# Kernel optimization log

Hardware: AMD Instinct MI355X
Metric: run time of the kernel (lower is better)

Reference implementation:

```python
import jax, jax.numpy as jnp
import numpy as np

N, E, G = 100000, 300000, 4096
ND, ED, H, ZI, ZS, NE, L = 64, 16, 256, 128, 128, 8, 3
LAMBDA_GRL = 1.0


def setup_inputs() -> dict:
    key = jax.random.key(0)
    ks = iter(jax.random.split(key, 64))
    def nrm(shape, scale=0.05):
        return jax.random.normal(next(ks), shape, jnp.float32) * scale
    inp = {
        'x': jax.random.normal(next(ks), (N, ND), jnp.float32),
        'edge_index': jax.random.randint(next(ks), (2, E), 0, N),
        'edge_attr': jax.random.normal(next(ks), (E, ED), jnp.float32),
        'batch': jnp.sort(jax.random.randint(next(ks), (N,), 0, G)),
        'node_W': nrm((ND, H)), 'node_b': nrm((H,)),
        'conv_eps': jnp.zeros((L,), jnp.float32),
        'edge_W': nrm((L, ED, H)), 'edge_b': nrm((L, H)),
        'mlp_W1': nrm((L, H, H)), 'mlp_b1': nrm((L, H)),
        'mlp_W2': nrm((L, H, H)), 'mlp_b2': nrm((L, H)),
        'gn_w': jnp.ones((L, H), jnp.float32), 'gn_b': jnp.zeros((L, H), jnp.float32),
        'gn_ms': jnp.ones((L, H), jnp.float32),
        'finv_W1': nrm((H, ZI)), 'finv_b1': nrm((ZI,)),
        'finv_W2': nrm((ZI, ZI)), 'finv_b2': nrm((ZI,)),
        'fspu_W1': nrm((H, ZS)), 'fspu_b1': nrm((ZS,)),
        'fspu_W2': nrm((ZS, ZS)), 'fspu_b2': nrm((ZS,)),
        'pred_W1': nrm((ZI, ZI)), 'pred_b1': nrm((ZI,)),
        'pred_W2': nrm((ZI, 1)), 'pred_b2': nrm((1,)),
        'adv_W1': nrm((ZI, ZI)), 'adv_b1': nrm((ZI,)),
        'adv_W2': nrm((ZI, NE)), 'adv_b2': nrm((NE,)),
    }
    return inp


def _mlp2(h, W1, b1, W2, b2):
    return jax.nn.relu(h @ W1 + b1) @ W2 + b2


def reference(x, edge_index, edge_attr, batch, node_W, node_b, conv_eps,
              edge_W, edge_b, mlp_W1, mlp_b1, mlp_W2, mlp_b2,
              gn_w, gn_b, gn_ms,
              finv_W1, finv_b1, finv_W2, finv_b2,
              fspu_W1, fspu_b1, fspu_W2, fspu_b2,
              pred_W1, pred_b1, pred_W2, pred_b2,
              adv_W1, adv_b1, adv_W2, adv_b2):
    src, dst = edge_index[0], edge_index[1]
    cnt = jax.ops.segment_sum(jnp.ones((N, 1), jnp.float32), batch, num_segments=G)
    cnt = jnp.maximum(cnt, 1.0)
    h = x @ node_W + node_b  # [N,H]
    for l in range(L):
        # GINEConv: sum_j relu(x_j + lin(e_ij))
        e = edge_attr @ edge_W[l] + edge_b[l]            # [E,H]
        m = jax.nn.relu(h[src] + e)                      # [E,H]
        agg = jax.ops.segment_sum(m, dst, num_segments=N)
        h = _mlp2((1.0 + conv_eps[l]) * h + agg, mlp_W1[l], mlp_b1[l], mlp_W2[l], mlp_b2[l])
        # GraphNorm
        mean = jax.ops.segment_sum(h, batch, num_segments=G) / cnt  # [G,H]
        out = h - gn_ms[l] * mean[batch]
        var = jax.ops.segment_sum(out * out, batch, num_segments=G) / cnt
        h = out * jax.lax.rsqrt(var[batch] + 1e-5) * gn_w[l] + gn_b[l]
        h = jax.nn.relu(h)  # dropout is identity at eval
    hg = jax.ops.segment_sum(h, batch, num_segments=G) / cnt  # global_mean_pool [G,H]
    z_inv = _mlp2(hg, finv_W1, finv_b1, finv_W2, finv_b2)
    z_spu = _mlp2(hg, fspu_W1, fspu_b1, fspu_W2, fspu_b2)
    yhat = _mlp2(z_inv, pred_W1, pred_b1, pred_W2, pred_b2)[:, 0]
    # gradient reversal: identity fwd, -lambda on bwd
    grl = jax.lax.stop_gradient(z_inv) * (1.0 + LAMBDA_GRL) - LAMBDA_GRL * z_inv
    envhat = _mlp2(grl, adv_W1, adv_b1, adv_W2, adv_b2)
    return (hg, z_inv, z_spu, yhat, envhat)
```

## Files before the change

kernel.cpp:

```cpp
#include <hip/hip_runtime.h>
#include <hip/hip_bf16.h>

typedef __bf16 bf16_t;
typedef __bf16 bf16x8 __attribute__((ext_vector_type(8)));
typedef __bf16 bf16x4 __attribute__((ext_vector_type(4)));
typedef float  f32x4  __attribute__((ext_vector_type(4)));

static constexpr int N_NODES = 100000;
static constexpr int N_EDGES = 300000;
static constexpr int N_GRAPH = 4096;
static constexpr int H  = 256;
static constexpr int ND = 64;
static constexpr int ZIC = 128;
static constexpr int NE = 8;
static constexpr int SCAN_B = 1024;

__device__ __forceinline__ int clampi(int v, int lo, int hi) {
  return v < lo ? lo : (v > hi ? hi : v);
}

__device__ __forceinline__ void dma16(const bf16_t* g, bf16_t* lds_base) {
  __builtin_amdgcn_global_load_lds(
      (const __attribute__((address_space(1))) void*)g,
      (__attribute__((address_space(3))) void*)lds_base, 16, 0, 0);
}

__global__ void compute_starts_kernel(const int* __restrict__ batch,
                                      int* __restrict__ starts,
                                      int* __restrict__ counts,
                                      int* __restrict__ cursor, int N, int G) {
  int i = blockIdx.x * blockDim.x + threadIdx.x;
  if (i >= N) return;
  counts[i] = 0;
  cursor[i] = 0;
  int b = clampi(batch[i], 0, G - 1);
  if (i == 0) {
    for (int g = 0; g <= b; ++g) starts[g] = 0;
  } else {
    int p = clampi(batch[i - 1], 0, G - 1);
    for (int g = p + 1; g <= b; ++g) starts[g] = i;
  }
  if (i == N - 1) {
    for (int g = b + 1; g <= G; ++g) starts[g] = N;
  }
}

__global__ void count_deg_kernel(const int* __restrict__ dst, int* __restrict__ counts, int E, int N) {
  int e = blockIdx.x * blockDim.x + threadIdx.x;
  if (e < E) atomicAdd(&counts[clampi(dst[e], 0, N - 1)], 1);
}

__global__ __launch_bounds__(SCAN_B) void scan1_kernel(const int* __restrict__ counts,
                                                       int* __restrict__ offs,
                                                       int* __restrict__ bsum, int N) {
  __shared__ int tmp[SCAN_B];
  int i = blockIdx.x * SCAN_B + threadIdx.x;
  int v = (i < N) ? counts[i] : 0;
  tmp[threadIdx.x] = v;
  __syncthreads();
  for (int d = 1; d < SCAN_B; d <<= 1) {
    int t = (threadIdx.x >= d) ? tmp[threadIdx.x - d] : 0;
    __syncthreads();
    tmp[threadIdx.x] += t;
    __syncthreads();
  }
  if (i < N) offs[i + 1] = tmp[threadIdx.x];
  if (threadIdx.x == SCAN_B - 1) bsum[blockIdx.x] = tmp[SCAN_B - 1];
  if (i == 0) offs[0] = 0;
}

__global__ void scan2_kernel(int* __restrict__ bsum, int nblk) {
  if (blockIdx.x == 0 && threadIdx.x == 0) {
    int run = 0;
    for (int b = 0; b < nblk; ++b) { int v = bsum[b]; bsum[b] = run; run += v; }
  }
}

__global__ __launch_bounds__(SCAN_B) void scan3_kernel(int* __restrict__ offs,
                                                       const int* __restrict__ bsum, int N) {
  int i = blockIdx.x * SCAN_B + threadIdx.x;
  if (i < N) offs[i + 1] += bsum[blockIdx.x];
}

__global__ void fill_scatter_kernel(const int* __restrict__ src, const int* __restrict__ dst,
                                    const float* __restrict__ eattr,
                                    const int* __restrict__ offs, int* __restrict__ cursor,
                                    int* __restrict__ src_srt, bf16_t* __restrict__ eat16,
                                    int E, int N) {
  int e = blockIdx.x * blockDim.x + threadIdx.x;
  if (e >= E) return;
  int d = clampi(dst[e], 0, N - 1);
  int pos = offs[d] + atomicAdd(&cursor[d], 1);
  if ((unsigned)pos >= (unsigned)E) return;
  int s = src[e];
  src_srt[pos] = ((unsigned)s < (unsigned)N_NODES) ? s : 0;
  const float* ea = eattr + (size_t)e * 16;
  union { bf16_t b[16]; uint4 u[2]; } pk;
#pragma unroll
  for (int k = 0; k < 16; ++k) pk.b[k] = (bf16_t)ea[k];
  uint4* dst16 = (uint4*)(eat16 + ((size_t)pos << 4));
  dst16[0] = pk.u[0];
  dst16[1] = pk.u[1];
}

__global__ void build_ewt16_kernel(const float* __restrict__ edge_W,
                                   bf16_t* __restrict__ ewt) {
  int idx = blockIdx.x * blockDim.x + threadIdx.x;
  if (idx >= 3 * 256 * 16) return;
  int l = idx / (256 * 16);
  int rem = idx - l * 256 * 16;
  int n = rem >> 4, k = rem & 15;
  ewt[idx] = (bf16_t)edge_W[(size_t)l * 16 * 256 + k * 256 + n];
}

__global__ void transpose_kernel(const float* __restrict__ W,
                                 bf16_t* __restrict__ Wt, int K, int Nc,
                                 size_t srcStride, size_t dstStride) {
  __shared__ float tile[32][33];
  const float* Wz = W + (size_t)blockIdx.z * srcStride;
  bf16_t* Wtz = Wt + (size_t)blockIdx.z * dstStride;
  int n0 = blockIdx.x * 32, k0 = blockIdx.y * 32;
  int tx = threadIdx.x, ty = threadIdx.y;
  for (int i = ty; i < 32; i += 8)
    tile[i][tx] = Wz[(size_t)(k0 + i) * Nc + n0 + tx];
  __syncthreads();
  for (int i = ty; i < 32; i += 8)
    Wtz[(size_t)(n0 + i) * K + k0 + tx] = (bf16_t)tile[tx][i];
}

__device__ __forceinline__ void load8_to_lds(const bf16_t* p, bool valid, uint4* dst) {
  uint4 v = make_uint4(0u, 0u, 0u, 0u);
  if (valid) v = *(const uint4*)p;
  *dst = v;
}
__device__ __forceinline__ void load8_to_lds(const float* p, bool valid, uint4* dst) {
  float4 f0 = make_float4(0.f, 0.f, 0.f, 0.f), f1 = f0;
  if (valid) { f0 = *(const float4*)p; f1 = *(const float4*)(p + 4); }
  union { bf16_t b[8]; uint4 u; } pk;
  pk.b[0] = (bf16_t)f0.x; pk.b[1] = (bf16_t)f0.y;
  pk.b[2] = (bf16_t)f0.z; pk.b[3] = (bf16_t)f0.w;
  pk.b[4] = (bf16_t)f1.x; pk.b[5] = (bf16_t)f1.y;
  pk.b[6] = (bf16_t)f1.z; pk.b[7] = (bf16_t)f1.w;
  *dst = pk.u;
}

template<int K, bool RELU, bool OUTF32, typename TIN>
__global__ __launch_bounds__(256) void gemm128_kernel(
    const TIN* __restrict__ U, const bf16_t* __restrict__ Wt,
    const float* __restrict__ bias, void* __restrict__ Out, int M, int Nc) {
  constexpr int LDT = 72;
  __shared__ bf16_t Ut[128 * LDT];
  __shared__ bf16_t Wl[128 * LDT];
  const int m0 = blockIdx.x * 128;
  const int n0 = blockIdx.y * 128;
  const int t = threadIdx.x;
  const int lane = t & 63;
  const int wave = t >> 6;
  const int wm = (wave >> 1) * 64;
  const int wn = (wave & 1) * 64;
  const int srow = t >> 1;
  const int sk = (t & 1) * 32;
  const int lr = lane & 15;
  const int lq = lane >> 4;
  const bool aok = (m0 + srow) < M;
  f32x4 acc[4][4] = {};

  for (int k0 = 0; k0 < K; k0 += 64) {
    const TIN* up = U + (size_t)(m0 + srow) * K + k0 + sk;
    const bf16_t* wp = Wt + (size_t)(n0 + srow) * K + k0 + sk;
#pragma unroll
    for (int q = 0; q < 4; ++q) {
      load8_to_lds(up + q * 8, aok, (uint4*)&Ut[srow * LDT + sk + q * 8]);
      load8_to_lds(wp + q * 8, true, (uint4*)&Wl[srow * LDT + sk + q * 8]);
    }
    __syncthreads();
#pragma unroll
    for (int s = 0; s < 2; ++s) {
      bf16x8 a[4], b[4];
#pragma unroll
      for (int mt = 0; mt < 4; ++mt)
        a[mt] = *(const bf16x8*)(&Ut[(wm + mt * 16 + lr) * LDT + s * 32 + lq * 8]);
#pragma unroll
      for (int nt = 0; nt < 4; ++nt)
        b[nt] = *(const bf16x8*)(&Wl[(wn + nt * 16 + lr) * LDT + s * 32 + lq * 8]);
#pragma unroll
      for (int mt = 0; mt < 4; ++mt)
#pragma unroll
        for (int nt = 0; nt < 4; ++nt)
          acc[mt][nt] = __builtin_amdgcn_mfma_f32_16x16x32_bf16(
              a[mt], b[nt], acc[mt][nt], 0, 0, 0);
    }
    __syncthreads();
  }

#pragma unroll
  for (int mt = 0; mt < 4; ++mt)
#pragma unroll
    for (int nt = 0; nt < 4; ++nt) {
      int col = n0 + wn + nt * 16 + lr;
      float bcol = bias[col];
#pragma unroll
      for (int r = 0; r < 4; ++r) {
        int row = m0 + wm + mt * 16 + lq * 4 + r;
        if (row < M) {
          float vv = acc[mt][nt][r] + bcol;
          if (RELU) vv = vv > 0.f ? vv : 0.f;
          if (OUTF32) ((float*)Out)[(size_t)row * Nc + col] = vv;
          else        ((bf16_t*)Out)[(size_t)row * Nc + col] = (bf16_t)vv;
        }
      }
    }
}

template<int K, bool RELU, bool OUTF32, typename TIN>
__global__ __launch_bounds__(256) void gemm64x2_kernel(
    const TIN* __restrict__ U0, const bf16_t* __restrict__ Wt0,
    const float* __restrict__ b0, void* __restrict__ O0,
    const TIN* __restrict__ U1, const bf16_t* __restrict__ Wt1,
    const float* __restrict__ b1, void* __restrict__ O1, int M, int Nc) {
  constexpr int LDT = 72;
  __shared__ bf16_t Ut[64 * LDT];
  __shared__ bf16_t Wl[64 * LDT];
  const TIN*    U    = blockIdx.z ? U1 : U0;
  const bf16_t* Wt   = blockIdx.z ? Wt1 : Wt0;
  const float*  bias = blockIdx.z ? b1 : b0;
  void*         Out  = blockIdx.z ? O1 : O0;
  const int m0 = blockIdx.x * 64;
  const int n0 = blockIdx.y * 64;
  const int t = threadIdx.x;
  const int lane = t & 63;
  const int wave = t >> 6;
  const int wm = (wave >> 1) * 32;
  const int wn = (wave & 1) * 32;
  const int srow = t >> 2;
  const int sk = (t & 3) * 8;
  const int lr = lane & 15;
  const int lq = lane >> 4;
  const bool aok = (m0 + srow) < M;
  f32x4 acc[2][2] = {};

  for (int k0 = 0; k0 < K; k0 += 64) {
    const TIN* up = U + (size_t)(m0 + srow) * K + k0 + sk;
    const bf16_t* wp = Wt + (size_t)(n0 + srow) * K + k0 + sk;
    load8_to_lds(up,      aok, (uint4*)&Ut[srow * LDT + sk]);
    load8_to_lds(up + 32, aok, (uint4*)&Ut[srow * LDT + sk + 32]);
    load8_to_lds(wp,      true, (uint4*)&Wl[srow * LDT + sk]);
    load8_to_lds(wp + 32, true, (uint4*)&Wl[srow * LDT + sk + 32]);
    __syncthreads();
#pragma unroll
    for (int s = 0; s < 2; ++s) {
      bf16x8 a[2], b[2];
#pragma unroll
      for (int mt = 0; mt < 2; ++mt)
        a[mt] = *(const bf16x8*)(&Ut[(wm + mt * 16 + lr) * LDT + s * 32 + lq * 8]);
#pragma unroll
      for (int nt = 0; nt < 2; ++nt)
        b[nt] = *(const bf16x8*)(&Wl[(wn + nt * 16 + lr) * LDT + s * 32 + lq * 8]);
#pragma unroll
      for (int mt = 0; mt < 2; ++mt)
#pragma unroll
        for (int nt = 0; nt < 2; ++nt)
          acc[mt][nt] = __builtin_amdgcn_mfma_f32_16x16x32_bf16(
              a[mt], b[nt], acc[mt][nt], 0, 0, 0);
    }
    __syncthreads();
  }

#pragma unroll
  for (int mt = 0; mt < 2; ++mt)
#pragma unroll
    for (int nt = 0; nt < 2; ++nt) {
      int col = n0 + wn + nt * 16 + lr;
      float bcol = bias[col];
#pragma unroll
      for (int r = 0; r < 4; ++r) {
        int row = m0 + wm + mt * 16 + lq * 4 + r;
        if (row < M) {
          float vv = acc[mt][nt][r] + bcol;
          if (RELU) vv = vv > 0.f ? vv : 0.f;
          if (OUTF32) ((float*)Out)[(size_t)row * Nc + col] = vv;
          else        ((bf16_t*)Out)[(size_t)row * Nc + col] = (bf16_t)vv;
        }
      }
    }
}

template<int K, bool RELU, bool OUTF32>
__global__ __launch_bounds__(256) void gemm128_dma_kernel(
    const bf16_t* __restrict__ U, const bf16_t* __restrict__ Wt,
    const float* __restrict__ bias, void* __restrict__ Out, int M, int Nc) {
  __shared__ bf16_t Ut[128 * 64];
  __shared__ bf16_t Wl[128 * 64];
  const int t = threadIdx.x;
  const int lane = t & 63;
  const int wave = t >> 6;
  const int m0 = blockIdx.x * 128;
  const int n0 = blockIdx.y * 128;
  const int wm = (wave >> 1) * 64;
  const int wn = (wave & 1) * 64;
  const int lr = lane & 15;
  const int lq = lane >> 4;
  const int subrow = wave * 8 + (lane >> 3);
  const int lchunk = (lane & 7) ^ (lane >> 3);
  f32x4 acc[4][4] = {};

  for (int k0 = 0; k0 < K; k0 += 64) {
#pragma unroll
    for (int q = 0; q < 4; ++q) {
      const int row = q * 32 + subrow;
      int urow = m0 + row; if (urow >= M) urow = M - 1;
      dma16(U + (size_t)urow * K + k0 + lchunk * 8, &Ut[(q * 32 + wave * 8) * 64]);
      dma16(Wt + (size_t)(n0 + row) * K + k0 + lchunk * 8, &Wl[(q * 32 + wave * 8) * 64]);
    }
    __syncthreads();
#pragma unroll
    for (int s = 0; s < 2; ++s) {
      bf16x8 a[4], b[4];
#pragma unroll
      for (int mt = 0; mt < 4; ++mt)
        a[mt] = *(const bf16x8*)(&Ut[(wm + mt * 16 + lr) * 64 + (((s * 4 + lq) ^ (lr & 7)) << 3)]);
#pragma unroll
      for (int nt = 0; nt < 4; ++nt)
        b[nt] = *(const bf16x8*)(&Wl[(wn + nt * 16 + lr) * 64 + (((s * 4 + lq) ^ (lr & 7)) << 3)]);
#pragma unroll
      for (int mt = 0; mt < 4; ++mt)
#pragma unroll
        for (int nt = 0; nt < 4; ++nt)
          acc[mt][nt] = __builtin_amdgcn_mfma_f32_16x16x32_bf16(
              a[mt], b[nt], acc[mt][nt], 0, 0, 0);
    }
    __syncthreads();
  }

#pragma unroll
  for (int mt = 0; mt < 4; ++mt)
#pragma unroll
    for (int nt = 0; nt < 4; ++nt) {
      int col = n0 + wn + nt * 16 + lr;
      float bcol = bias[col];
#pragma unroll
      for (int r = 0; r < 4; ++r) {
        int row = m0 + wm + mt * 16 + lq * 4 + r;
        if (row < M) {
          float vv = acc[mt][nt][r] + bcol;
          if (RELU) vv = vv > 0.f ? vv : 0.f;
          if (OUTF32) ((float*)Out)[(size_t)row * Nc + col] = vv;
          else        ((bf16_t*)Out)[(size_t)row * Nc + col] = (bf16_t)vv;
        }
      }
    }
}

__global__ __launch_bounds__(256) void gine_gather_mfma_kernel(
    const bf16_t* __restrict__ h, const bf16_t* __restrict__ eat16,
    const int* __restrict__ src_sorted, const int* __restrict__ offs,
    const bf16_t* __restrict__ ewt, const float* __restrict__ eb,
    const float* __restrict__ eps_p, bf16_t* __restrict__ u) {
  constexpr int HP = H + 8;
  __shared__ bf16_t slin[2][16 * HP];
  const int t = threadIdx.x;
  const int wave = t >> 6;
  const int lane = t & 63;
  const int lr = lane & 15;
  const int lq = lane >> 4;
  const int lane4 = lane * 4;
  const int n0 = blockIdx.x * 16;
  const int nodeB = n0 + wave * 4;

  bf16x4 hs[4];
#pragma unroll
  for (int k = 0; k < 4; ++k)
    hs[k] = *(const bf16x4*)(h + (size_t)(nodeB + k) * H + lane4);

  bf16x8 bfrag[4];
#pragma unroll
  for (int nt = 0; nt < 4; ++nt) {
    bf16x8 bv = {};
    if (lq < 2)
      bv = *(const bf16x8*)(ewt + ((wave * 64 + nt * 16 + lr) << 4) + (lq << 3));
    bfrag[nt] = bv;
  }
  float ebv[4];
#pragma unroll
  for (int i = 0; i < 4; ++i) ebv[i] = eb[lane4 + i];

  int bs = offs[n0], be = offs[n0 + 16];
  bs = clampi(bs, 0, N_EDGES);
  be = clampi(be, bs, N_EDGES);
  int nb[5];
#pragma unroll
  for (int q = 0; q < 5; ++q) nb[q] = offs[nodeB + q];
  nb[0] = clampi(nb[0], bs, be);
#pragma unroll
  for (int q = 1; q < 5; ++q) nb[q] = clampi(nb[q], nb[q - 1], be);

  f32x4 accv[4] = {};
  int parity = 0;

  for (int cb = bs; cb < be; cb += 16, parity ^= 1) {
    int arow = cb + lr;
    if (arow >= N_EDGES) arow = N_EDGES - 1;
    bf16x8 afrag = {};
    if (lq < 2)
      afrag = *(const bf16x8*)(eat16 + ((size_t)arow << 4) + (lq << 3));

    int j0p = nb[0] > cb ? nb[0] : cb;
    int j1p = nb[1] < cb + 16 ? nb[1] : cb + 16;
    int sidx[4];
    bf16x4 hv[4];
    if (j0p < j1p) {
#pragma unroll
      for (int q = 0; q < 4; ++q) {
        int jj = j0p + q; if (jj > j1p - 1) jj = j1p - 1;
        sidx[q] = src_sorted[jj];
      }
    }

    f32x4 c[4];
#pragma unroll
    for (int nt = 0; nt < 4; ++nt) {
      f32x4 z = {};
      c[nt] = __builtin_amdgcn_mfma_f32_16x16x32_bf16(afrag, bfrag[nt], z, 0, 0, 0);
    }
#pragma unroll
    for (int nt = 0; nt < 4; ++nt)
#pragma unroll
      for (int r = 0; r < 4; ++r)
        slin[parity][(lq * 4 + r) * HP + wave * 64 + nt * 16 + lr] = (bf16_t)c[nt][r];

    if (j0p < j1p) {
#pragma unroll
      for (int q = 0; q < 4; ++q)
        hv[q] = *(const bf16x4*)(h + (size_t)sidx[q] * H + lane4);
    }

    __syncthreads();

#pragma unroll
    for (int k = 0; k < 4; ++k) {
      int j0 = nb[k] > cb ? nb[k] : cb;
      int j1 = nb[k + 1] < cb + 16 ? nb[k + 1] : cb + 16;
      for (int jb = j0; jb < j1; jb += 4) {
        if (k != 0 || jb != j0p) {
#pragma unroll
          for (int q = 0; q < 4; ++q) {
            int jj = jb + q; if (jj > j1 - 1) jj = j1 - 1;
            sidx[q] = src_sorted[jj];
          }
#pragma unroll
          for (int q = 0; q < 4; ++q)
            hv[q] = *(const bf16x4*)(h + (size_t)sidx[q] * H + lane4);
        }
#pragma unroll
        for (int q = 0; q < 4; ++q) {
          if (jb + q < j1) {
            bf16x4 lv = *(const bf16x4*)(&slin[parity][(jb + q - cb) * HP + lane4]);
#pragma unroll
            for (int i = 0; i < 4; ++i)
              accv[k][i] += fmaxf((float)hv[q][i] + (float)lv[i] + ebv[i], 0.f);
          }
        }
      }
    }
  }

  const float sc = 1.0f + eps_p[0];
#pragma unroll
  for (int k = 0; k < 4; ++k) {
    union { bf16x4 v; uint2 b; } o;
#pragma unroll
    for (int i = 0; i < 4; ++i) o.v[i] = (bf16_t)(sc * (float)hs[k][i] + accv[k][i]);
    *(uint2*)(u + (size_t)(nodeB + k) * H + lane4) = o.b;
  }
}

__global__ __launch_bounds__(256) void graphnorm_kernel(
    const bf16_t* __restrict__ v, bf16_t* __restrict__ hout,
    const int* __restrict__ starts,
    const float* __restrict__ w, const float* __restrict__ b,
    const float* __restrict__ ms, float* __restrict__ hg) {
  constexpr int RS = 9;
  constexpr int PS = 13;
  __shared__ float red[4 * 64 * RS];
  __shared__ float prm[64 * PS];
  const int g = blockIdx.x;
  const int t = threadIdx.x;
  const int lane = t & 63;
  const int wave = t >> 6;
  const int c0 = lane * 4;
  int s = starts[g], e = starts[g + 1];
  s = clampi(s, 0, N_NODES);
  e = clampi(e, s, N_NODES);
  const float cnt = (float)((e - s) > 1 ? (e - s) : 1);

  float sx[4] = {0.f, 0.f, 0.f, 0.f}, sxx[4] = {0.f, 0.f, 0.f, 0.f};
  {
    int i = s + wave;
    for (; i + 4 < e; i += 8) {
      bf16x4 x0 = *(const bf16x4*)(v + (size_t)i * H + c0);
      bf16x4 x1 = *(const bf16x4*)(v + (size_t)(i + 4) * H + c0);
#pragma unroll
      for (int j = 0; j < 4; ++j) {
        float f0 = (float)x0[j], f1 = (float)x1[j];
        sx[j] += f0 + f1; sxx[j] += f0 * f0 + f1 * f1;
      }
    }
    if (i < e) {
      bf16x4 x0 = *(const bf16x4*)(v + (size_t)i * H + c0);
#pragma unroll
      for (int j = 0; j < 4; ++j) {
        float f0 = (float)x0[j];
        sx[j] += f0; sxx[j] += f0 * f0;
      }
    }
  }
  float* myred = &red[(wave * 64 + lane) * RS];
#pragma unroll
  for (int j = 0; j < 4; ++j) { myred[j] = sx[j]; myred[4 + j] = sxx[j]; }
  __syncthreads();

  if (wave == 0) {
#pragma unroll
    for (int j = 0; j < 4; ++j) {
      float fsx = red[lane * RS + j] + red[(64 + lane) * RS + j] +
                  red[(128 + lane) * RS + j] + red[(192 + lane) * RS + j];
      float fsxx = red[lane * RS + 4 + j] + red[(64 + lane) * RS + 4 + j] +
                   red[(128 + lane) * RS + 4 + j] + red[(192 + lane) * RS + 4 + j];
      float mean = fsx / cnt;
      float sub = ms[c0 + j] * mean;
      float var = fsxx / cnt - 2.f * sub * mean + sub * sub;
      var = fmaxf(var, 0.f);
      prm[lane * PS + j] = sub;
      prm[lane * PS + 4 + j] = rsqrtf(var + 1e-5f) * w[c0 + j];
      prm[lane * PS + 8 + j] = b[c0 + j];
    }
  }
  __syncthreads();
  float sub[4], inv[4], bb[4];
#pragma unroll
  for (int j = 0; j < 4; ++j) {
    sub[j] = prm[lane * PS + j];
    inv[j] = prm[lane * PS + 4 + j];
    bb[j] = prm[lane * PS + 8 + j];
  }

  float psum[4] = {0.f, 0.f, 0.f, 0.f};
  {
    int i = s + wave;
    for (; i + 4 < e; i += 8) {
      bf16x4 x0 = *(const bf16x4*)(v + (size_t)i * H + c0);
      bf16x4 x1 = *(const bf16x4*)(v + (size_t)(i + 4) * H + c0);
      union { bf16x4 o; uint2 u; } p0, p1;
#pragma unroll
      for (int j = 0; j < 4; ++j) {
        float o0 = ((float)x0[j] - sub[j]) * inv[j] + bb[j];
        float o1 = ((float)x1[j] - sub[j]) * inv[j] + bb[j];
        o0 = o0 > 0.f ? o0 : 0.f;
        o1 = o1 > 0.f ? o1 : 0.f;
        psum[j] += o0 + o1;
        p0.o[j] = (bf16_t)o0; p1.o[j] = (bf16_t)o1;
      }
      *(uint2*)(hout + (size_t)i * H + c0) = p0.u;
      *(uint2*)(hout + (size_t)(i + 4) * H + c0) = p1.u;
    }
    if (i < e) {
      bf16x4 x0 = *(const bf16x4*)(v + (size_t)i * H + c0);
      union { bf16x4 o; uint2 u; } p0;
#pragma unroll
      for (int j = 0; j < 4; ++j) {
        float o0 = ((float)x0[j] - sub[j]) * inv[j] + bb[j];
        o0 = o0 > 0.f ? o0 : 0.f;
        psum[j] += o0;
        p0.o[j] = (bf16_t)o0;
      }
      *(uint2*)(hout + (size_t)i * H + c0) = p0.u;
    }
  }

  if (hg) {
#pragma unroll
    for (int j = 0; j < 4; ++j) myred[j] = psum[j];
    __syncthreads();
    if (wave == 0) {
#pragma unroll
      for (int j = 0; j < 4; ++j) {
        float p = red[lane * RS + j] + red[(64 + lane) * RS + j] +
                  red[(128 + lane) * RS + j] + red[(192 + lane) * RS + j];
        hg[(size_t)g * H + c0 + j] = p / cnt;
      }
    }
  }
}

__global__ void head_out2_kernel(const bf16_t* __restrict__ In1, const float* __restrict__ W1,
                                 const float* __restrict__ b1, float* __restrict__ O1,
                                 const bf16_t* __restrict__ In2, const float* __restrict__ W2,
                                 const float* __restrict__ b2, float* __restrict__ O2,
                                 int M) {
  int idx = blockIdx.x * blockDim.x + threadIdx.x;
  if (idx < M) {
    float acc = b1[0];
    const bf16_t* in = In1 + (size_t)idx * ZIC;
    for (int k = 0; k < ZIC; ++k) acc += (float)in[k] * W1[k];
    O1[idx] = acc;
  } else {
    int j = idx - M;
    if (j >= M * NE) return;
    int r = j >> 3, n = j & 7;
    float acc = b2[n];
    const bf16_t* in = In2 + (size_t)r * ZIC;
    for (int k = 0; k < ZIC; ++k) acc += (float)in[k] * W2[(size_t)k * NE + n];
    O2[j] = acc;
  }
}

extern "C" void kernel_launch(void* const* d_in, const int* in_sizes, int n_in,
                              void* d_out, int out_size, void* d_ws, size_t ws_size,
                              hipStream_t stream) {
  (void)in_sizes; (void)n_in; (void)out_size; (void)ws_size;
  const float* x        = (const float*)d_in[0];
  const int*   eidx     = (const int*)d_in[1];
  const float* eattr    = (const float*)d_in[2];
  const int*   batch    = (const int*)d_in[3];
  const float* node_W   = (const float*)d_in[4];
  const float* node_b   = (const float*)d_in[5];
  const float* conv_eps = (const float*)d_in[6];
  const float* edge_W   = (const float*)d_in[7];
  const float* edge_b   = (const float*)d_in[8];
  const float* mlp_W1   = (const float*)d_in[9];
  const float* mlp_b1   = (const float*)d_in[10];
  const float* mlp_W2   = (const float*)d_in[11];
  const float* mlp_b2   = (const float*)d_in[12];
  const float* gn_w     = (const float*)d_in[13];
  const float* gn_b     = (const float*)d_in[14];
  const float* gn_ms    = (const float*)d_in[15];
  const float* finv_W1  = (const float*)d_in[16];
  const float* finv_b1  = (const float*)d_in[17];
  const float* finv_W2  = (const float*)d_in[18];
  const float* finv_b2  = (const float*)d_in[19];
  const float* fspu_W1  = (const float*)d_in[20];
  const float* fspu_b1  = (const float*)d_in[21];
  const float* fspu_W2  = (const float*)d_in[22];
  const float* fspu_b2  = (const float*)d_in[23];
  const float* pred_W1  = (const float*)d_in[24];
  const float* pred_b1  = (const float*)d_in[25];
  const float* pred_W2  = (const float*)d_in[26];
  const float* pred_b2  = (const float*)d_in[27];
  const float* adv_W1   = (const float*)d_in[28];
  const float* adv_b1   = (const float*)d_in[29];
  const float* adv_W2   = (const float*)d_in[30];
  const float* adv_b2   = (const float*)d_in[31];
  float* out = (float*)d_out;

  float* out_hg = out;
  float* out_zi = out + (size_t)N_GRAPH * H;
  float* out_zs = out_zi + (size_t)N_GRAPH * ZIC;
  float* out_yh = out_zs + (size_t)N_GRAPH * ZIC;
  float* out_ev = out_yh + N_GRAPH;

  char* wp = (char*)d_ws;
  auto alloc = [&](size_t bytes) { char* p = wp; wp += (bytes + 255) & ~(size_t)255; return p; };
  bf16_t* A        = (bf16_t*)alloc((size_t)N_NODES * H * 2);
  bf16_t* B        = (bf16_t*)alloc((size_t)N_NODES * H * 2);
  bf16_t* Wt       = (bf16_t*)alloc((size_t)(H * ND + 6 * H * H) * 2);
  bf16_t* WtH      = (bf16_t*)alloc((size_t)(2 * ZIC * H + 4 * ZIC * ZIC) * 2);
  bf16_t* ewt16    = (bf16_t*)alloc((size_t)3 * 256 * 16 * 2);
  bf16_t* eat16    = (bf16_t*)alloc((size_t)N_EDGES * 16 * 2);
  int*    starts   = (int*)alloc((size_t)(N_GRAPH + 1) * 4);
  int*    counts   = (int*)alloc((size_t)N_NODES * 4);
  int*    cursor   = (int*)alloc((size_t)N_NODES * 4);
  int*    offs     = (int*)alloc((size_t)(N_NODES + 1) * 4);
  int*    bsum     = (int*)alloc((size_t)SCAN_B * 4);
  int*    src_srt  = (int*)alloc((size_t)N_EDGES * 4);
  bf16_t* tmp1     = (bf16_t*)alloc((size_t)N_GRAPH * ZIC * 2);
  bf16_t* tmp2     = (bf16_t*)alloc((size_t)N_GRAPH * ZIC * 2);

  const int* srcp = eidx;
  const int* dstp = eidx + N_EDGES;
  const int nscan = (N_NODES + SCAN_B - 1) / SCAN_B;

  compute_starts_kernel<<<(N_NODES + 255) / 256, 256, 0, stream>>>(
      batch, starts, counts, cursor, N_NODES, N_GRAPH);
  count_deg_kernel<<<(N_EDGES + 255) / 256, 256, 0, stream>>>(dstp, counts, N_EDGES, N_NODES);
  scan1_kernel<<<nscan, SCAN_B, 0, stream>>>(counts, offs, bsum, N_NODES);
  scan2_kernel<<<1, 64, 0, stream>>>(bsum, nscan);
  scan3_kernel<<<nscan, SCAN_B, 0, stream>>>(offs, bsum, N_NODES);
  fill_scatter_kernel<<<(N_EDGES + 255) / 256, 256, 0, stream>>>(
      srcp, dstp, eattr, offs, cursor, src_srt, eat16, N_EDGES, N_NODES);
  build_ewt16_kernel<<<(3 * 256 * 16 + 255) / 256, 256, 0, stream>>>(edge_W, ewt16);

  bf16_t* WtN = Wt;
  bf16_t* Wt1base = Wt + H * ND;
  bf16_t* Wt2base = Wt + H * ND + (size_t)H * H;
  auto Wt1l = [&](int l) { return Wt1base + (size_t)(2 * l) * H * H; };
  auto Wt2l = [&](int l) { return Wt2base + (size_t)(2 * l) * H * H; };
  transpose_kernel<<<dim3(H / 32, ND / 32, 1), dim3(32, 8), 0, stream>>>(node_W, WtN, ND, H, 0, 0);
  transpose_kernel<<<dim3(H / 32, H / 32, 3), dim3(32, 8), 0, stream>>>(
      mlp_W1, Wt1base, H, H, (size_t)H * H, (size_t)2 * H * H);
  transpose_kernel<<<dim3(H / 32, H / 32, 3), dim3(32, 8), 0, stream>>>(
      mlp_W2, Wt2base, H, H, (size_t)H * H, (size_t)2 * H * H);

  bf16_t* fT1 = WtH;
  bf16_t* fT2 = fT1 + ZIC * H;
  bf16_t* sT1 = fT2 + ZIC * ZIC;
  bf16_t* sT2 = sT1 + ZIC * H;
  bf16_t* pT1 = sT2 + ZIC * ZIC;
  bf16_t* aT1 = pT1 + ZIC * ZIC;
  transpose_kernel<<<dim3(ZIC / 32, H / 32, 1), dim3(32, 8), 0, stream>>>(finv_W1, fT1, H, ZIC, 0, 0);
  transpose_kernel<<<dim3(ZIC / 32, ZIC / 32, 1), dim3(32, 8), 0, stream>>>(finv_W2, fT2, ZIC, ZIC, 0, 0);
  transpose_kernel<<<dim3(ZIC / 32, H / 32, 1), dim3(32, 8), 0, stream>>>(fspu_W1, sT1, H, ZIC, 0, 0);
  transpose_kernel<<<dim3(ZIC / 32, ZIC / 32, 1), dim3(32, 8), 0, stream>>>(fspu_W2, sT2, ZIC, ZIC, 0, 0);
  transpose_kernel<<<dim3(ZIC / 32, ZIC / 32, 1), dim3(32, 8), 0, stream>>>(pred_W1, pT1, ZIC, ZIC, 0, 0);
  transpose_kernel<<<dim3(ZIC / 32, ZIC / 32, 1), dim3(32, 8), 0, stream>>>(adv_W1, aT1, ZIC, ZIC, 0, 0);

  dim3 ggrid((N_NODES + 127) / 128, H / 128);
  gemm128_kernel<ND, false, false><<<ggrid, 256, 0, stream>>>(x, WtN, node_b, A, N_NODES, H);

  for (int l = 0; l < 3; ++l) {
    gine_gather_mfma_kernel<<<N_NODES / 16, 256, 0, stream>>>(
        A, eat16, src_srt, offs, ewt16 + (size_t)l * 256 * 16,
        edge_b + l * H, conv_eps + l, B);
    gemm128_dma_kernel<H, true,  false><<<ggrid, 256, 0, stream>>>(B, Wt1l(l), mlp_b1 + l * H, A, N_NODES, H);
    gemm128_dma_kernel<H, false, false><<<ggrid, 256, 0, stream>>>(A, Wt2l(l), mlp_b2 + l * H, B, N_NODES, H);
    graphnorm_kernel<<<N_GRAPH, 256, 0, stream>>>(B, A, starts, gn_w + l * H, gn_b + l * H,
                                                  gn_ms + l * H, (l == 2) ? out_hg : nullptr);
  }

  dim3 hgrid2(N_GRAPH / 64, ZIC / 64, 2);
  gemm64x2_kernel<H, true, false, float><<<hgrid2, 256, 0, stream>>>(
      out_hg, fT1, finv_b1, tmp1, out_hg, sT1, fspu_b1, tmp2, N_GRAPH, ZIC);
  gemm64x2_kernel<ZIC, false, true, bf16_t><<<hgrid2, 256, 0, stream>>>(
      tmp1, fT2, finv_b2, out_zi, tmp2, sT2, fspu_b2, out_zs, N_GRAPH, ZIC);
  gemm64x2_kernel<ZIC, true, false, float><<<hgrid2, 256, 0, stream>>>(
      out_zi, pT1, pred_b1, tmp1, out_zi, aT1, adv_b1, tmp2, N_GRAPH, ZIC);
  head_out2_kernel<<<(N_GRAPH * (1 + NE) + 255) / 256, 256, 0, stream>>>(
      tmp1, pred_W2, pred_b2, out_yh, tmp2, adv_W2, adv_b2, out_ev, N_GRAPH);
}
```

Measured before the change: 836.8 us.

## Make GINE gather per-wave independent, removing block-wide syncs via per-wave edge-linear LDS

Each wave now computes the full 256-wide edge linear projection for its own 4 nodes' edge range into a private LDS slice, so the block-wide __syncthreads per 16-edge chunk disappears and waves iterate only over their own edges. The edge weight table is permuted so each lane's MFMA output columns land contiguously and can be packed into 8-byte LDS stores. The cost is four times as many MFMAs per wave (the full H instead of a quarter), B fragments reloaded from global/L1 each chunk, and more LDS.

```diff
diff --git a/kernel.cpp b/kernel.cpp
--- a/kernel.cpp
+++ b/kernel.cpp
@@ -109,8 +109,9 @@
   if (idx >= 3 * 256 * 16) return;
   int l = idx / (256 * 16);
   int rem = idx - l * 256 * 16;
-  int n = rem >> 4, k = rem & 15;
-  ewt[idx] = (bf16_t)edge_W[(size_t)l * 16 * 256 + k * 256 + n];
+  int s = rem >> 4, k = rem & 15;
+  int ch = ((s & 15) << 4) | (s >> 4);
+  ewt[idx] = (bf16_t)edge_W[(size_t)l * 16 * 256 + k * 256 + ch];
 }
 
 __global__ void transpose_kernel(const float* __restrict__ W,
@@ -356,85 +357,76 @@
     const int* __restrict__ src_sorted, const int* __restrict__ offs,
     const bf16_t* __restrict__ ewt, const float* __restrict__ eb,
     const float* __restrict__ eps_p, bf16_t* __restrict__ u) {
-  constexpr int HP = H + 8;
-  __shared__ bf16_t slin[2][16 * HP];
+  constexpr int HPS = 264;
+  __shared__ bf16_t slin[4][16 * HPS];
   const int t = threadIdx.x;
   const int wave = t >> 6;
   const int lane = t & 63;
   const int lr = lane & 15;
   const int lq = lane >> 4;
   const int lane4 = lane * 4;
-  const int n0 = blockIdx.x * 16;
-  const int nodeB = n0 + wave * 4;
+  const int nodeB = blockIdx.x * 16 + wave * 4;
+  bf16_t* sl = &slin[wave][0];
 
   bf16x4 hs[4];
 #pragma unroll
   for (int k = 0; k < 4; ++k)
     hs[k] = *(const bf16x4*)(h + (size_t)(nodeB + k) * H + lane4);
 
-  bf16x8 bfrag[4];
-#pragma unroll
-  for (int nt = 0; nt < 4; ++nt) {
-    bf16x8 bv = {};
-    if (lq < 2)
-      bv = *(const bf16x8*)(ewt + ((wave * 64 + nt * 16 + lr) << 4) + (lq << 3));
-    bfrag[nt] = bv;
-  }
   float ebv[4];
 #pragma unroll
   for (int i = 0; i < 4; ++i) ebv[i] = eb[lane4 + i];
 
-  int bs = offs[n0], be = offs[n0 + 16];
-  bs = clampi(bs, 0, N_EDGES);
-  be = clampi(be, bs, N_EDGES);
   int nb[5];
 #pragma unroll
   for (int q = 0; q < 5; ++q) nb[q] = offs[nodeB + q];
-  nb[0] = clampi(nb[0], bs, be);
-#pragma unroll
-  for (int q = 1; q < 5; ++q) nb[q] = clampi(nb[q], nb[q - 1], be);
+  nb[0] = clampi(nb[0], 0, N_EDGES);
+#pragma unroll
+  for (int q = 1; q < 5; ++q) nb[q] = clampi(nb[q], nb[q - 1], N_EDGES);
 
   f32x4 accv[4] = {};
-  int parity = 0;
-
-  for (int cb = bs; cb < be; cb += 16, parity ^= 1) {
+
+  for (int cb = nb[0]; cb < nb[4]; cb += 16) {
+    int j0p = nb[0] > cb ? nb[0] : cb;
+    int j1p = nb[1] < cb + 16 ? nb[1] : cb + 16;
+    int sidx[4];
+    bf16x4 hv[4];
+    if (j0p < j1p) {
+#pragma unroll
+      for (int q = 0; q < 4; ++q) {
+        int jj = j0p + q; if (jj > j1p - 1) jj = j1p - 1;
+        sidx[q] = src_sorted[jj];
+      }
+#pragma unroll
+      for (int q = 0; q < 4; ++q)
+        hv[q] = *(const bf16x4*)(h + (size_t)sidx[q] * H + lane4);
+    }
+
     int arow = cb + lr;
     if (arow >= N_EDGES) arow = N_EDGES - 1;
     bf16x8 afrag = {};
     if (lq < 2)
       afrag = *(const bf16x8*)(eat16 + ((size_t)arow << 4) + (lq << 3));
 
-    int j0p = nb[0] > cb ? nb[0] : cb;
-    int j1p = nb[1] < cb + 16 ? nb[1] : cb + 16;
-    int sidx[4];
-    bf16x4 hv[4];
-    if (j0p < j1p) {
-#pragma unroll
-      for (int q = 0; q < 4; ++q) {
-        int jj = j0p + q; if (jj > j1p - 1) jj = j1p - 1;
-        sidx[q] = src_sorted[jj];
-      }
-    }
-
-    f32x4 c[4];
-#pragma unroll
-    for (int nt = 0; nt < 4; ++nt) {
-      f32x4 z = {};
-      c[nt] = __builtin_amdgcn_mfma_f32_16x16x32_bf16(afrag, bfrag[nt], z, 0, 0, 0);
-    }
-#pragma unroll
-    for (int nt = 0; nt < 4; ++nt)
-#pragma unroll
-      for (int r = 0; r < 4; ++r)
-        slin[parity][(lq * 4 + r) * HP + wave * 64 + nt * 16 + lr] = (bf16_t)c[nt][r];
-
-    if (j0p < j1p) {
-#pragma unroll
-      for (int q = 0; q < 4; ++q)
-        hv[q] = *(const bf16x4*)(h + (size_t)sidx[q] * H + lane4);
-    }
-
-    __syncthreads();
+#pragma unroll
+    for (int g = 0; g < 4; ++g) {
+      f32x4 c4[4];
+#pragma unroll
+      for (int j = 0; j < 4; ++j) {
+        bf16x8 bv = {};
+        if (lq < 2)
+          bv = *(const bf16x8*)(ewt + (((g * 4 + j) * 16 + lr) << 4) + (lq << 3));
+        f32x4 z = {};
+        c4[j] = __builtin_amdgcn_mfma_f32_16x16x32_bf16(afrag, bv, z, 0, 0, 0);
+      }
+#pragma unroll
+      for (int r = 0; r < 4; ++r) {
+        union { bf16_t b[4]; uint2 u2; } pk;
+#pragma unroll
+        for (int j = 0; j < 4; ++j) pk.b[j] = (bf16_t)c4[j][r];
+        *(uint2*)(sl + (lq * 4 + r) * HPS + lr * 16 + g * 4) = pk.u2;
+      }
+    }
 
 #pragma unroll
     for (int k = 0; k < 4; ++k) {
@@ -454,7 +446,7 @@
 #pragma unroll
         for (int q = 0; q < 4; ++q) {
           if (jb + q < j1) {
-            bf16x4 lv = *(const bf16x4*)(&slin[parity][(jb + q - cb) * HP + lane4]);
+            bf16x4 lv = *(const bf16x4*)(sl + (jb + q - cb) * HPS + lane4);
 #pragma unroll
             for (int i = 0; i < 4; ++i)
               accv[k][i] += fmaxf((float)hv[q][i] + (float)lv[i] + ebv[i], 0.f);
```

New measurement: 817.7 us. 1.02x faster.
